# Kernel optimization log

Hardware: AMD Instinct MI355X
Metric: run time of the kernel (lower is better)

## Reference

```python
import jax, jax.numpy as jnp
import numpy as np

# sign with straight-through estimator: grad passes only where |input| < 1
@jax.custom_vjp
def sign_ste(x):
    return jnp.sign(x)

def _sign_ste_fwd(x):
    return jnp.sign(x), x

def _sign_ste_bwd(x, g):
    return (jnp.where(jnp.abs(x) < 1.0, g, jnp.zeros_like(g)),)

sign_ste.defvjp(_sign_ste_fwd, _sign_ste_bwd)

# weight binarization: torch mutates weight.data in-place, so autograd treats
# sign() as identity w.r.t. the weight variable (plain linear gradient)
@jax.custom_vjp
def sign_id(w):
    return jnp.sign(w)

def _sign_id_fwd(w):
    return jnp.sign(w), None

def _sign_id_bwd(_, g):
    return (g,)

sign_id.defvjp(_sign_id_fwd, _sign_id_bwd)


def setup_inputs() -> dict:
    key = jax.random.key(0)
    k1, k2, k3 = jax.random.split(key, 3)
    x = jax.random.normal(k1, (8192, 4096), dtype=jnp.float32)
    # weight initialized to random ±1 (bernoulli(0.5)*2-1), as in __init__
    W = jnp.sign(jax.random.normal(k2, (4096, 4096), dtype=jnp.float32))
    b = jax.random.normal(k3, (4096,), dtype=jnp.float32) * 0.02
    return {"x": x, "W": W, "b": b}


def reference(x, W, b):
    # x: [N, in]; W: [out, in]; b: [out]
    x_mean = jnp.mean(jnp.abs(x))          # scalar scale, differentiable
    xb = sign_ste(x)                        # ±1 activations, STE gradient
    wb = sign_id(W)                         # ±1 weights, identity gradient
    out = jnp.einsum('ni,oi->no', xb, wb) + b  # [N, out]
    return out * x_mean
```

## Files before the change

### kernel.cpp

```cpp
#include <hip/hip_runtime.h>

typedef int intx4 __attribute__((ext_vector_type(4)));
typedef int intx8 __attribute__((ext_vector_type(8)));
typedef float floatx4 __attribute__((ext_vector_type(4)));

#define M_DIM 8192
#define N_DIM 4096
#define K_DIM 4096
#define KB2 (K_DIM / 2)

#define PACK_BLOCKS 2048
#define NF4_X ((size_t)M_DIM * K_DIM / 4)
#define NF4_TOT (NF4_X + (size_t)N_DIM * K_DIM / 4)

__device__ __forceinline__ void gld_lds16(const char* g, char* l) {
  __builtin_amdgcn_global_load_lds(
      (const __attribute__((address_space(1))) unsigned int*)g,
      (__attribute__((address_space(3))) unsigned int*)l,
      16, 0, 0);
}

__device__ __forceinline__ unsigned nib(float v) {
  return v > 0.0f ? 0x2u : (v < 0.0f ? 0xAu : 0x0u);
}

__global__ __launch_bounds__(256) void pack_kernel(const float* __restrict__ x,
                                                   const float* __restrict__ Wm,
                                                   unsigned short* __restrict__ pk,
                                                   double* __restrict__ accd) {
  const int t = threadIdx.x;
  const size_t stride = (size_t)PACK_BLOCKS * 256;
  const float4* __restrict__ X4 = (const float4*)x;
  const float4* __restrict__ W4 = (const float4*)Wm;
  float s = 0.0f;
  for (size_t i = (size_t)blockIdx.x * 256 + t; i < NF4_TOT; i += stride) {
    float4 v;
    if (i < NF4_X) {
      v = X4[i];
      s += fabsf(v.x) + fabsf(v.y) + fabsf(v.z) + fabsf(v.w);
    } else {
      v = W4[i - NF4_X];
    }
    pk[i] = (unsigned short)(nib(v.x) | (nib(v.y) << 4) | (nib(v.z) << 8) |
                             (nib(v.w) << 12));
  }
  #pragma unroll
  for (int off = 32; off > 0; off >>= 1) s += __shfl_down(s, off);
  __shared__ float sp[4];
  if ((t & 63) == 0) sp[t >> 6] = s;
  __syncthreads();
  if (t == 0) atomicAdd(accd, (double)(sp[0] + sp[1] + sp[2] + sp[3]));
}

__global__ __launch_bounds__(512, 2) void gemm_kernel(const char* __restrict__ Xb,
                                                      const char* __restrict__ Wb,
                                                      const float* __restrict__ bias,
                                                      const double* __restrict__ accd,
                                                      float* __restrict__ out) {
  __shared__ __align__(16) char lA[4][16384];
  __shared__ __align__(16) char lB[4][16384];
  const int t = threadIdx.x;
  const int lane = t & 63;
  const int w = t >> 6;
  const int m16 = lane & 15;
  const int quad = lane >> 4;
  const int bM = blockIdx.y * 256;
  const int bN = blockIdx.x * 256;
  const int waveM = (w >> 2) * 128;
  const int waveN = (w & 3) * 64;

  const int srl = 2 * (t >> 3) + (t & 1);
  const int ssc = (t >> 1) & 3;
  const int g0 = (ssc + (srl >> 1)) & 3;
  const char* gA = Xb + (size_t)(bM + srl) * KB2 + g0 * 16;
  const char* gB = Wb + (size_t)(bN + srl) * KB2 + g0 * 16;
  const int ldst = w * 1024;

  int offA[8], offB[4];
  #pragma unroll
  for (int i = 0; i < 8; ++i) {
    const int m = waveM + i * 16 + m16;
    offA[i] = (m >> 1) * 128 + (((quad - (m >> 1)) & 3)) * 32 + (m & 1) * 16;
  }
  #pragma unroll
  for (int j = 0; j < 4; ++j) {
    const int n = waveN + j * 16 + m16;
    offB[j] = (n >> 1) * 128 + (((quad - (n >> 1)) & 3)) * 32 + (n & 1) * 16;
  }

  floatx4 acc[8][4];
  #pragma unroll
  for (int i = 0; i < 8; ++i)
    #pragma unroll
    for (int j = 0; j < 4; ++j)
      acc[i][j] = (floatx4){0.0f, 0.0f, 0.0f, 0.0f};

#define STAGE(BUF, TILE)                                                    \
  do {                                                                      \
    const size_t kb = (size_t)(TILE) * 64;                                  \
    gld_lds16(gA + kb, &lA[BUF][ldst]);                                     \
    gld_lds16(gA + kb + (size_t)128 * KB2, &lA[BUF][8192 + ldst]);          \
    gld_lds16(gB + kb, &lB[BUF][ldst]);                                     \
    gld_lds16(gB + kb + (size_t)128 * KB2, &lB[BUF][8192 + ldst]);          \
  } while (0)

#define COMPUTE(BUF)                                                        \
  do {                                                                      \
    intx8 b8[4];                                                            \
    _Pragma("unroll")                                                       \
    for (int j = 0; j < 4; ++j) {                                           \
      intx4 lo = *(const intx4*)&lB[BUF][offB[j]];                          \
      b8[j] = (intx8){lo[0], lo[1], lo[2], lo[3], 0, 0, 0, 0};              \
    }                                                                       \
    __builtin_amdgcn_s_setprio(1);                                          \
    _Pragma("unroll")                                                       \
    for (int i = 0; i < 8; ++i) {                                           \
      intx4 lo = *(const intx4*)&lA[BUF][offA[i]];                          \
      intx8 a8 = (intx8){lo[0], lo[1], lo[2], lo[3], 0, 0, 0, 0};           \
      _Pragma("unroll")                                                     \
      for (int j = 0; j < 4; ++j)                                           \
        acc[i][j] = __builtin_amdgcn_mfma_scale_f32_16x16x128_f8f6f4(       \
            a8, b8[j], acc[i][j], 4, 4, 0, 0x7F7F7F7F, 0, 0x7F7F7F7F);      \
    }                                                                       \
    __builtin_amdgcn_s_setprio(0);                                          \
  } while (0)

#define WAITV(N) asm volatile("s_waitcnt vmcnt(" #N ")" ::: "memory")
#define FENCE() asm volatile("" ::: "memory")
#define BAR() __builtin_amdgcn_s_barrier()

  STAGE(0, 0);
  STAGE(1, 1);
  STAGE(2, 2);

  for (int b = 0; b < 28; b += 4) {
    STAGE(3, b + 3); WAITV(12); BAR(); FENCE(); COMPUTE(0); FENCE(); BAR();
    STAGE(0, b + 4); WAITV(12); BAR(); FENCE(); COMPUTE(1); FENCE(); BAR();
    STAGE(1, b + 5); WAITV(12); BAR(); FENCE(); COMPUTE(2); FENCE(); BAR();
    STAGE(2, b + 6); WAITV(12); BAR(); FENCE(); COMPUTE(3); FENCE(); BAR();
  }
  STAGE(3, 31); WAITV(12); BAR(); FENCE(); COMPUTE(0); FENCE(); BAR();
  WAITV(8);  BAR(); FENCE(); COMPUTE(1); FENCE(); BAR();
  WAITV(4);  BAR(); FENCE(); COMPUTE(2); FENCE(); BAR();
  WAITV(0);  BAR(); FENCE(); COMPUTE(3);
#undef STAGE
#undef COMPUTE
#undef WAITV
#undef FENCE
#undef BAR

  const float scale = (float)(*accd * (1.0 / (double)((size_t)M_DIM * K_DIM)));

  #pragma unroll
  for (int j = 0; j < 4; ++j) {
    const int col = bN + waveN + j * 16 + m16;
    const float bj = bias[col];
    #pragma unroll
    for (int i = 0; i < 8; ++i) {
      const size_t row0 = (size_t)(bM + waveM + i * 16 + quad * 4);
      float* po = out + row0 * N_DIM + col;
      #pragma unroll
      for (int r = 0; r < 4; ++r)
        po[(size_t)r * N_DIM] = (acc[i][j][r] + bj) * scale;
    }
  }
}

extern "C" void kernel_launch(void* const* d_in, const int* in_sizes, int n_in,
                              void* d_out, int out_size, void* d_ws, size_t ws_size,
                              hipStream_t stream) {
  const float* x = (const float*)d_in[0];
  const float* W = (const float*)d_in[1];
  const float* b = (const float*)d_in[2];
  float* out = (float*)d_out;

  double* accd = (double*)d_ws;
  char* Xb = (char*)d_ws + 256;
  char* Wb = (char*)d_ws + 256 + (size_t)M_DIM * K_DIM / 2;

  hipMemsetAsync(d_ws, 0, 8, stream);
  pack_kernel<<<PACK_BLOCKS, 256, 0, stream>>>(x, W, (unsigned short*)Xb, accd);
  gemm_kernel<<<dim3(N_DIM / 256, M_DIM / 256), 512, 0, stream>>>(Xb, Wb, b, accd, out);
}
```

Baseline: 352.2 us.

## Interleave staged loads with MFMA sub-blocks using triple-buffered LDS pipeline

```diff
diff --git a/kernel.cpp b/kernel.cpp
--- a/kernel.cpp
+++ b/kernel.cpp
@@ -57,8 +57,8 @@
                                                       const float* __restrict__ bias,
                                                       const double* __restrict__ accd,
                                                       float* __restrict__ out) {
-  __shared__ __align__(16) char lA[4][16384];
-  __shared__ __align__(16) char lB[4][16384];
+  __shared__ __align__(16) char lA[3][16384];
+  __shared__ __align__(16) char lB[3][16384];
   const int t = threadIdx.x;
   const int lane = t & 63;
   const int w = t >> 6;
@@ -95,59 +95,93 @@
     for (int j = 0; j < 4; ++j)
       acc[i][j] = (floatx4){0.0f, 0.0f, 0.0f, 0.0f};
 
-#define STAGE(BUF, TILE)                                                    \
-  do {                                                                      \
-    const size_t kb = (size_t)(TILE) * 64;                                  \
-    gld_lds16(gA + kb, &lA[BUF][ldst]);                                     \
-    gld_lds16(gA + kb + (size_t)128 * KB2, &lA[BUF][8192 + ldst]);          \
-    gld_lds16(gB + kb, &lB[BUF][ldst]);                                     \
-    gld_lds16(gB + kb + (size_t)128 * KB2, &lB[BUF][8192 + ldst]);          \
+#define WAITV4() asm volatile("s_waitcnt vmcnt(4)" ::: "memory")
+#define WAITV0() asm volatile("s_waitcnt vmcnt(0)" ::: "memory")
+#define BARF()                                  \
+  do {                                          \
+    __builtin_amdgcn_s_barrier();               \
+    asm volatile("" ::: "memory");              \
   } while (0)
 
-#define COMPUTE(BUF)                                                        \
-  do {                                                                      \
-    intx8 b8[4];                                                            \
-    _Pragma("unroll")                                                       \
-    for (int j = 0; j < 4; ++j) {                                           \
-      intx4 lo = *(const intx4*)&lB[BUF][offB[j]];                          \
-      b8[j] = (intx8){lo[0], lo[1], lo[2], lo[3], 0, 0, 0, 0};              \
-    }                                                                       \
-    __builtin_amdgcn_s_setprio(1);                                          \
-    _Pragma("unroll")                                                       \
-    for (int i = 0; i < 8; ++i) {                                           \
-      intx4 lo = *(const intx4*)&lA[BUF][offA[i]];                          \
-      intx8 a8 = (intx8){lo[0], lo[1], lo[2], lo[3], 0, 0, 0, 0};           \
-      _Pragma("unroll")                                                     \
-      for (int j = 0; j < 4; ++j)                                           \
-        acc[i][j] = __builtin_amdgcn_mfma_scale_f32_16x16x128_f8f6f4(       \
-            a8, b8[j], acc[i][j], 4, 4, 0, 0x7F7F7F7F, 0, 0x7F7F7F7F);      \
-    }                                                                       \
-    __builtin_amdgcn_s_setprio(0);                                          \
+#define MM2(I0, L0, L1)                                                      \
+  do {                                                                       \
+    intx8 a0_ = (intx8){(L0)[0], (L0)[1], (L0)[2], (L0)[3], 0, 0, 0, 0};     \
+    intx8 a1_ = (intx8){(L1)[0], (L1)[1], (L1)[2], (L1)[3], 0, 0, 0, 0};     \
+    __builtin_amdgcn_s_setprio(1);                                           \
+    _Pragma("unroll")                                                        \
+    for (int j = 0; j < 4; ++j) {                                            \
+      acc[I0][j] = __builtin_amdgcn_mfma_scale_f32_16x16x128_f8f6f4(         \
+          a0_, b8[j], acc[I0][j], 4, 4, 0, 0x7F7F7F7F, 0, 0x7F7F7F7F);       \
+      acc[(I0) + 1][j] = __builtin_amdgcn_mfma_scale_f32_16x16x128_f8f6f4(   \
+          a1_, b8[j], acc[(I0) + 1][j], 4, 4, 0, 0x7F7F7F7F, 0, 0x7F7F7F7F); \
+    }                                                                        \
+    __builtin_amdgcn_s_setprio(0);                                           \
   } while (0)
 
-#define WAITV(N) asm volatile("s_waitcnt vmcnt(" #N ")" ::: "memory")
-#define FENCE() asm volatile("" ::: "memory")
-#define BAR() __builtin_amdgcn_s_barrier()
-
-  STAGE(0, 0);
-  STAGE(1, 1);
-  STAGE(2, 2);
-
-  for (int b = 0; b < 28; b += 4) {
-    STAGE(3, b + 3); WAITV(12); BAR(); FENCE(); COMPUTE(0); FENCE(); BAR();
-    STAGE(0, b + 4); WAITV(12); BAR(); FENCE(); COMPUTE(1); FENCE(); BAR();
-    STAGE(1, b + 5); WAITV(12); BAR(); FENCE(); COMPUTE(2); FENCE(); BAR();
-    STAGE(2, b + 6); WAITV(12); BAR(); FENCE(); COMPUTE(3); FENCE(); BAR();
-  }
-  STAGE(3, 31); WAITV(12); BAR(); FENCE(); COMPUTE(0); FENCE(); BAR();
-  WAITV(8);  BAR(); FENCE(); COMPUTE(1); FENCE(); BAR();
-  WAITV(4);  BAR(); FENCE(); COMPUTE(2); FENCE(); BAR();
-  WAITV(0);  BAR(); FENCE(); COMPUTE(3);
-#undef STAGE
-#undef COMPUTE
-#undef WAITV
-#undef FENCE
-#undef BAR
+#define ITER(BUF, NXT, TILE, DOSTG, WMODE)                                   \
+  do {                                                                       \
+    intx8 b8[4];                                                             \
+    {                                            \
+      _Pragma("unroll")                                                      \
+      for (int j = 0; j < 4; ++j) {                                          \
+        intx4 lo = *(const intx4*)&lB[BUF][offB[j]];                         \
+        b8[j] = (intx8){lo[0], lo[1], lo[2], lo[3], 0, 0, 0, 0};             \
+      }                                                                      \
+      intx4 l0 = *(const intx4*)&lA[BUF][offA[0]];                           \
+      intx4 l1 = *(const intx4*)&lA[BUF][offA[1]];                           \
+      if (DOSTG) gld_lds16(gA + (size_t)(TILE) * 64, &lA[NXT][ldst]);        \
+      BARF(); MM2(0, l0, l1); BARF();                                        \
+    }                                                                        \
+    {                                                    \
+      intx4 l0 = *(const intx4*)&lA[BUF][offA[2]];                           \
+      intx4 l1 = *(const intx4*)&lA[BUF][offA[3]];                           \
+      if (DOSTG)                                                             \
+        gld_lds16(gA + (size_t)(TILE) * 64 + (size_t)128 * KB2,              \
+                  &lA[NXT][8192 + ldst]);                                    \
+      BARF(); MM2(2, l0, l1); BARF();                                        \
+    }                                                                        \
+    {                                                    \
+      intx4 l0 = *(const intx4*)&lA[BUF][offA[4]];                           \
+      intx4 l1 = *(const intx4*)&lA[BUF][offA[5]];                           \
+      if (DOSTG) gld_lds16(gB + (size_t)(TILE) * 64, &lB[NXT][ldst]);        \
+      BARF(); MM2(4, l0, l1); BARF();                                        \
+    }                                                                        \
+    {                           \
+      intx4 l0 = *(const intx4*)&lA[BUF][offA[6]];                           \
+      intx4 l1 = *(const intx4*)&lA[BUF][offA[7]];                           \
+      if (DOSTG)                                                             \
+        gld_lds16(gB + (size_t)(TILE) * 64 + (size_t)128 * KB2,              \
+                  &lB[NXT][8192 + ldst]);                                    \
+      if ((WMODE) == 0) WAITV4();                                            \
+      else if ((WMODE) == 1) WAITV0();                                       \
+      BARF(); MM2(6, l0, l1); BARF();                                        \
+    }                                                                        \
+  } while (0)
+
+  gld_lds16(gA + (size_t)0 * 64, &lA[0][ldst]);
+  gld_lds16(gA + (size_t)0 * 64 + (size_t)128 * KB2, &lA[0][8192 + ldst]);
+  gld_lds16(gB + (size_t)0 * 64, &lB[0][ldst]);
+  gld_lds16(gB + (size_t)0 * 64 + (size_t)128 * KB2, &lB[0][8192 + ldst]);
+  gld_lds16(gA + (size_t)1 * 64, &lA[1][ldst]);
+  gld_lds16(gA + (size_t)1 * 64 + (size_t)128 * KB2, &lA[1][8192 + ldst]);
+  gld_lds16(gB + (size_t)1 * 64, &lB[1][ldst]);
+  gld_lds16(gB + (size_t)1 * 64 + (size_t)128 * KB2, &lB[1][8192 + ldst]);
+  WAITV4();
+  BARF();
+
+  for (int g = 0; g < 10; ++g) {
+    const int t3 = g * 3;
+    ITER(0, 2, t3 + 2, 1, 0);
+    ITER(1, 0, t3 + 3, 1, 0);
+    ITER(2, 1, t3 + 4, 1, 0);
+  }
+  ITER(0, 2, 0, 0, 1);
+  ITER(1, 0, 0, 0, 2);
+#undef ITER
+#undef MM2
+#undef WAITV4
+#undef WAITV0
+#undef BARF
 
   const float scale = (float)(*accd * (1.0 / (double)((size_t)M_DIM * K_DIM)));
 
```

Result: no change. 357.6 us (+1.6%).
